# Kernel optimization log

Measured on AMD Instinct MI355X. Metric: run time of the kernel, lower is better.

Reference implementation:

```python
import jax, jax.numpy as jnp
import numpy as np

N_NODES = 50000
N_EDGES = 800000
IN_DIM = 128
HID = 128
NUM_CLASSES = 2


def setup_inputs() -> dict:
    key = jax.random.key(0)
    ks = jax.random.split(key, 16)
    inp = {
        "adj_row": jax.random.randint(ks[0], (N_EDGES,), 0, N_NODES),
        "adj_col": jax.random.randint(ks[1], (N_EDGES,), 0, N_NODES),
        "adj_vals": jax.random.uniform(ks[2], (N_EDGES,), dtype=jnp.float32),
        "input_feature": jax.random.normal(ks[3], (N_NODES, IN_DIM), dtype=jnp.float32),
        "graph_indicator": jax.random.randint(ks[4], (N_NODES,), 0, 64),
        # GCN layer params (kaiming-uniform-ish init; zeros bias like the torch module)
        "W1": jax.random.uniform(ks[5], (IN_DIM, HID), jnp.float32, -1, 1) * np.sqrt(6.0 / IN_DIM),
        "b1": jnp.zeros((HID,), jnp.float32),
        "W2": jax.random.uniform(ks[6], (HID, HID), jnp.float32, -1, 1) * np.sqrt(6.0 / HID),
        "b2": jnp.zeros((HID,), jnp.float32),
        "W3": jax.random.uniform(ks[7], (HID, HID), jnp.float32, -1, 1) * np.sqrt(6.0 / HID),
        "b3": jnp.zeros((HID,), jnp.float32),
        # fc params (torch.nn.Linear default init range)
        "fcW1": jax.random.uniform(ks[8], (3 * HID, HID), jnp.float32, -1, 1) / np.sqrt(3 * HID),
        "fcb1": jax.random.uniform(ks[9], (HID,), jnp.float32, -1, 1) / np.sqrt(3 * HID),
        "fcW2": jax.random.uniform(ks[10], (HID, HID // 2), jnp.float32, -1, 1) / np.sqrt(HID),
        "fcb2": jax.random.uniform(ks[11], (HID // 2,), jnp.float32, -1, 1) / np.sqrt(HID),
        "fcW3": jax.random.uniform(ks[12], (HID // 2, NUM_CLASSES), jnp.float32, -1, 1) / np.sqrt(HID // 2),
        "fcb3": jax.random.uniform(ks[13], (NUM_CLASSES,), jnp.float32, -1, 1) / np.sqrt(HID // 2),
    }
    return inp


def _gcn_layer(row, col, vals, x, W, b, n_nodes):
    # support = X @ W  -> dense GEMM
    support = x @ W
    # sparse.mm(A, support): out[i] = sum_{e: row[e]=i} vals[e] * support[col[e]]
    msgs = support[col] * vals[:, None]  # [E, D] gather + scale
    agg = jax.ops.segment_sum(msgs, row, num_segments=n_nodes)
    return agg + b


def reference(adj_row, adj_col, adj_vals, input_feature, graph_indicator,
              W1, b1, W2, b2, W3, b3, fcW1, fcb1, fcW2, fcb2, fcW3, fcb3):
    n = input_feature.shape[0]
    g1 = jax.nn.relu(_gcn_layer(adj_row, adj_col, adj_vals, input_feature, W1, b1, n))
    g2 = jax.nn.relu(_gcn_layer(adj_row, adj_col, adj_vals, g1, W2, b2, n))
    g3 = jax.nn.relu(_gcn_layer(adj_row, adj_col, adj_vals, g2, W3, b3, n))
    feat = jnp.concatenate([g1, g2, g3], axis=1)  # [N, 3*HID]
    h = jax.nn.relu(feat @ fcW1 + fcb1)
    h = jax.nn.relu(h @ fcW2 + fcb2)
    logits = h @ fcW3 + fcb3
    return logits
```

## Files before the change

### kernel.cpp

```cpp
#include <hip/hip_runtime.h>
#include <hip/hip_bf16.h>

#define N_NODES 50000
#define N_EDGES 800000
#define NB16 3125
#define BCAP16 448
#define REG16 560

static inline int cdiv(int a, int b) { return (a + b - 1) / b; }

typedef __attribute__((ext_vector_type(8))) short short8;
typedef __attribute__((ext_vector_type(4))) float f32x4;

__device__ __forceinline__ float b2f(unsigned short u) {
    union { unsigned int i; float f; } c;
    c.i = ((unsigned int)u) << 16;
    return c.f;
}
__device__ __forceinline__ unsigned short f2bb(float f) {
    __hip_bfloat16 h = __float2bfloat16(f);
    return *(unsigned short*)&h;
}

__device__ __forceinline__ void pack_one(const float* __restrict__ W,
                                         __hip_bfloat16* __restrict__ out,
                                         int K, int N, int t) {
    int lane = t & 63;
    int kc = (t >> 6) % (K / 32);
    int nt = (t >> 6) / (K / 32);
    int kbase = kc * 32 + (lane >> 4) * 8;
    int col = nt * 16 + (lane & 15);
    __hip_bfloat16* dst = out + (size_t)t * 8;
#pragma unroll
    for (int j = 0; j < 8; ++j)
        dst[j] = __float2bfloat16(W[(size_t)(kbase + j) * N + col]);
}

__global__ __launch_bounds__(256)
void stage1_kernel(const int* __restrict__ row, const int* __restrict__ col,
                   const float* __restrict__ vals, int* __restrict__ bcursor,
                   int2* __restrict__ tmp, int E,
                   const float* __restrict__ x, __hip_bfloat16* __restrict__ support,
                   int M,
                   const float* __restrict__ W1, const float* __restrict__ W2,
                   const float* __restrict__ W3, const float* __restrict__ fcW1,
                   const float* __restrict__ fcW2,
                   __hip_bfloat16* __restrict__ pW2, __hip_bfloat16* __restrict__ pW3,
                   __hip_bfloat16* __restrict__ pfcW1, __hip_bfloat16* __restrict__ pfcW2) {
    __shared__ union {
        unsigned short As[64][136];
        struct { int hist[NB16]; int base[NB16]; } bin;
    } sh;
    const int b = blockIdx.x;
    const int tid = threadIdx.x;

    if (b < 196) {
        const int CH = 4096;
        int e0 = b * CH;
        for (int i = tid; i < NB16; i += 256) sh.bin.hist[i] = 0;
        __syncthreads();
        for (int i = tid; i < CH; i += 256) {
            int e = e0 + i;
            if (e < E) atomicAdd(&sh.bin.hist[row[e] >> 4], 1);
        }
        __syncthreads();
        for (int i = tid; i < NB16; i += 256) {
            int c = sh.bin.hist[i];
            sh.bin.base[i] = (c > 0) ? (i * BCAP16 + atomicAdd(&bcursor[i], c)) : 0;
            sh.bin.hist[i] = 0;
        }
        __syncthreads();
        for (int i = tid; i < CH; i += 256) {
            int e = e0 + i;
            if (e < E) {
                int r = row[e];
                int bk = r >> 4;
                int rk = atomicAdd(&sh.bin.hist[bk], 1);
                tmp[sh.bin.base[bk] + rk] = make_int2(((r & 15) << 16) | col[e],
                                                      __float_as_int(vals[e]));
            }
        }
        return;
    }

    if (b < 978) {
        const int wave = tid >> 6;
        const int lane = tid & 63;
        const int ln15 = lane & 15;
        const int quad = lane >> 4;
        const int m0 = (b - 196) * 64;

        short8 bfr[4][2];
#pragma unroll
        for (int kc = 0; kc < 4; ++kc)
#pragma unroll
            for (int h = 0; h < 2; ++h)
#pragma unroll
                for (int j = 0; j < 8; ++j)
                    bfr[kc][h][j] = (short)f2bb(
                        W1[(size_t)(kc * 32 + quad * 8 + j) * 128 + (wave * 2 + h) * 16 + ln15]);

#pragma unroll
        for (int i = 0; i < 4; ++i) {
            int idx = tid + i * 256;
            int r = idx >> 4;
            int c8 = (idx & 15) * 8;
            uint4 pk = {0, 0, 0, 0};
            if (m0 + r < M) {
                const float* src = &x[(size_t)(m0 + r) * 128 + c8];
                float4 a = *(const float4*)src;
                float4 bq = *(const float4*)(src + 4);
                pk.x = f2bb(a.x) | ((unsigned int)f2bb(a.y) << 16);
                pk.y = f2bb(a.z) | ((unsigned int)f2bb(a.w) << 16);
                pk.z = f2bb(bq.x) | ((unsigned int)f2bb(bq.y) << 16);
                pk.w = f2bb(bq.z) | ((unsigned int)f2bb(bq.w) << 16);
            }
            *(uint4*)&sh.As[r][c8] = pk;
        }
        __syncthreads();

        f32x4 acc[4][2];
#pragma unroll
        for (int s = 0; s < 4; ++s)
#pragma unroll
            for (int h = 0; h < 2; ++h) acc[s][h] = (f32x4){0.f, 0.f, 0.f, 0.f};
#pragma unroll
        for (int kc = 0; kc < 4; ++kc) {
            short8 af[4];
#pragma unroll
            for (int s = 0; s < 4; ++s)
                af[s] = *(const short8*)&sh.As[s * 16 + ln15][kc * 32 + quad * 8];
#pragma unroll
            for (int s = 0; s < 4; ++s)
#pragma unroll
                for (int h = 0; h < 2; ++h)
                    acc[s][h] = __builtin_amdgcn_mfma_f32_16x16x32_bf16(
                        af[s], bfr[kc][h], acc[s][h], 0, 0, 0);
        }
#pragma unroll
        for (int s = 0; s < 4; ++s)
#pragma unroll
            for (int h = 0; h < 2; ++h) {
                int cl = (wave * 2 + h) * 16 + ln15;
#pragma unroll
                for (int r = 0; r < 4; ++r) {
                    int rw = m0 + s * 16 + quad * 4 + r;
                    if (rw < M)
                        support[(size_t)rw * 128 + cl] = __float2bfloat16(acc[s][h][r]);
                }
            }
        return;
    }

    int pb = b - 978;
    if (pb < 8)       pack_one(W2,  pW2,  128, 128, pb * 256 + tid);
    else if (pb < 16) pack_one(W3,  pW3,  128, 128, (pb - 8) * 256 + tid);
    else if (pb < 40) pack_one(fcW1, pfcW1, 384, 128, (pb - 16) * 256 + tid);
    else              pack_one(fcW2, pfcW2, 128, 64, (pb - 40) * 256 + tid);
}

__device__ __forceinline__ void accum8(float* acc, long long e, uint4 u) {
    float f = __int_as_float((int)(e >> 32));
    acc[0] += f * b2f((unsigned short)(u.x & 0xffff));
    acc[1] += f * b2f((unsigned short)(u.x >> 16));
    acc[2] += f * b2f((unsigned short)(u.y & 0xffff));
    acc[3] += f * b2f((unsigned short)(u.y >> 16));
    acc[4] += f * b2f((unsigned short)(u.z & 0xffff));
    acc[5] += f * b2f((unsigned short)(u.z >> 16));
    acc[6] += f * b2f((unsigned short)(u.w & 0xffff));
    acc[7] += f * b2f((unsigned short)(u.w >> 16));
}

__device__ __forceinline__ void agg_node(const long long* __restrict__ ep,
                                         const __hip_bfloat16* __restrict__ support,
                                         int p, int end, int g, int j, float* acc) {
#pragma unroll
    for (int k = 0; k < 8; ++k) acc[k] = 0.f;
    long long e0 = 0, e1 = 0;
    uint4 u0 = {0, 0, 0, 0}, u1 = {0, 0, 0, 0};
    bool have = false;
    if (p < end) {
        e0 = ep[p + g];
        e1 = ep[p + 4 + g];
        u0 = *(const uint4*)&support[(size_t)(unsigned int)(e0 & 0xffffffffu) * 128 + j * 8];
        u1 = *(const uint4*)&support[(size_t)(unsigned int)(e1 & 0xffffffffu) * 128 + j * 8];
        p += 8;
        have = true;
    }
    while (p < end) {
        long long f0 = ep[p + g];
        long long f1 = ep[p + 4 + g];
        uint4 w0 = *(const uint4*)&support[(size_t)(unsigned int)(f0 & 0xffffffffu) * 128 + j * 8];
        uint4 w1 = *(const uint4*)&support[(size_t)(unsigned int)(f1 & 0xffffffffu) * 128 + j * 8];
        accum8(acc, e0, u0);
        accum8(acc, e1, u1);
        e0 = f0; u0 = w0; e1 = f1; u1 = w1;
        p += 8;
    }
    if (have) {
        accum8(acc, e0, u0);
        accum8(acc, e1, u1);
    }
#pragma unroll
    for (int k = 0; k < 8; ++k) {
        acc[k] += __shfl_xor(acc[k], 16);
        acc[k] += __shfl_xor(acc[k], 32);
    }
}

__device__ __forceinline__ uint4 pack_row8(const float* acc, float4 b0, float4 b1) {
    unsigned int q0 = (unsigned int)f2bb(fmaxf(acc[0] + b0.x, 0.f))
                    | ((unsigned int)f2bb(fmaxf(acc[1] + b0.y, 0.f)) << 16);
    unsigned int q1 = (unsigned int)f2bb(fmaxf(acc[2] + b0.z, 0.f))
                    | ((unsigned int)f2bb(fmaxf(acc[3] + b0.w, 0.f)) << 16);
    unsigned int q2 = (unsigned int)f2bb(fmaxf(acc[4] + b1.x, 0.f))
                    | ((unsigned int)f2bb(fmaxf(acc[5] + b1.y, 0.f)) << 16);
    unsigned int q3 = (unsigned int)f2bb(fmaxf(acc[6] + b1.z, 0.f))
                    | ((unsigned int)f2bb(fmaxf(acc[7] + b1.w, 0.f)) << 16);
    return (uint4){q0, q1, q2, q3};
}

__global__ __launch_bounds__(256, 8)
void spmm_sort_gemm_kernel(const int2* __restrict__ tmp,
                           const int* __restrict__ bcursor,
                           int2* __restrict__ rowrange, int2* __restrict__ epack,
                           const __hip_bfloat16* __restrict__ support,
                           const float* __restrict__ bias,
                           __hip_bfloat16* __restrict__ gout,
                           const __hip_bfloat16* __restrict__ pW,
                           __hip_bfloat16* __restrict__ Cout,
                           int N) {
    __shared__ unsigned short As[16][136];
    __shared__ int cnt[16];
    __shared__ int cur[16];
    __shared__ int rpos[16];
    const int b = blockIdx.x;
    const int tid = threadIdx.x;
    const int wv = tid >> 6;
    const int l = tid & 63;
    const int g = l >> 4;
    const int j = l & 15;
    const int m0 = b * 16;
    const int r0 = m0;

    if (tid < 16) cnt[tid] = 0;
    __syncthreads();
    int slab = b * BCAP16;
    int send = slab + bcursor[b];
    for (int i = slab + tid; i < send; i += 256)
        atomicAdd(&cnt[tmp[i].x >> 16], 1);
    __syncthreads();
    if (tid == 0) {
        int pos = b * REG16;
#pragma unroll 1
        for (int k = 0; k < 16; ++k) {
            int rc = cnt[k];
            int pc = (rc + 7) & ~7;
            rpos[k] = pos;
            cur[k] = pos;
            rowrange[r0 + k] = make_int2(pos, pos + pc);
            pos += pc;
        }
    }
    __syncthreads();
    for (int i = slab + tid; i < send; i += 256) {
        int2 v = tmp[i];
        int rl = v.x >> 16;
        int pos = atomicAdd(&cur[rl], 1);
        epack[pos] = make_int2(v.x & 0xffff, v.y);
    }
    if (tid < 16) {
        int rc = cnt[tid];
        int pc = (rc + 7) & ~7;
        int pos = rpos[tid];
#pragma unroll 1
        for (int i = pos + rc; i < pos + pc; ++i)
            epack[i] = make_int2(0, 0);
    }
    __syncthreads();

    const long long* ep = (const long long*)epack;
    float4 b0 = *(const float4*)&bias[j * 8];
    float4 b1 = *(const float4*)&bias[j * 8 + 4];
    for (int i = 0; i < 4; ++i) {
        int i0 = wv * 4 + i;
        int ps = rpos[i0];
        int pe = ps + ((cnt[i0] + 7) & ~7);
        float acc[8];
        agg_node(ep, support, ps, pe, g, j, acc);
        if (g == 0) {
            uint4 st = pack_row8(acc, b0, b1);
            *(uint4*)&As[i0][j * 8] = st;
            *(uint4*)&gout[(size_t)(m0 + i0) * 384 + j * 8] = st;
        }
    }
    __syncthreads();

    const int ln15 = l & 15;
    const int quad = l >> 4;
    f32x4 acc2[2];
    acc2[0] = (f32x4){0.f, 0.f, 0.f, 0.f};
    acc2[1] = (f32x4){0.f, 0.f, 0.f, 0.f};
#pragma unroll
    for (int kc = 0; kc < 4; ++kc) {
        short8 af = *(const short8*)&As[ln15][kc * 32 + quad * 8];
#pragma unroll
        for (int h = 0; h < 2; ++h) {
            int nt = wv * 2 + h;
            short8 bf = *(const short8*)&pW[((size_t)(nt * 4 + kc) * 64 + l) * 8];
            acc2[h] = __builtin_amdgcn_mfma_f32_16x16x32_bf16(af, bf, acc2[h], 0, 0, 0);
        }
    }
#pragma unroll
    for (int h = 0; h < 2; ++h) {
        int cl = (wv * 2 + h) * 16 + ln15;
#pragma unroll
        for (int r = 0; r < 4; ++r) {
            int rw = m0 + quad * 4 + r;
            if (rw < N)
                Cout[(size_t)rw * 128 + cl] = __float2bfloat16(acc2[h][r]);
        }
    }
}

__global__ __launch_bounds__(256, 8)
void spmm_gemm_kernel(const int2* __restrict__ rowrange,
                      const int2* __restrict__ epack,
                      const __hip_bfloat16* __restrict__ support,
                      const float* __restrict__ bias,
                      __hip_bfloat16* __restrict__ gout,
                      const __hip_bfloat16* __restrict__ pW,
                      __hip_bfloat16* __restrict__ Cout,
                      int N) {
    __shared__ unsigned short As[16][136];
    const int tid = threadIdx.x;
    const int wv = tid >> 6;
    const int l = tid & 63;
    const int g = l >> 4;
    const int j = l & 15;
    const int m0 = blockIdx.x * 16;
    const long long* ep = (const long long*)epack;
    float4 b0 = *(const float4*)&bias[j * 8];
    float4 b1 = *(const float4*)&bias[j * 8 + 4];

    for (int i = 0; i < 4; ++i) {
        int node = m0 + wv * 4 + i;
        if (node < N) {
            int2 rr = rowrange[node];
            float acc[8];
            agg_node(ep, support, rr.x, rr.y, g, j, acc);
            if (g == 0) {
                uint4 st = pack_row8(acc, b0, b1);
                *(uint4*)&As[wv * 4 + i][j * 8] = st;
                *(uint4*)&gout[(size_t)node * 384 + j * 8] = st;
            }
        } else if (g == 0) {
            *(uint4*)&As[wv * 4 + i][j * 8] = (uint4){0, 0, 0, 0};
        }
    }
    __syncthreads();

    const int ln15 = l & 15;
    const int quad = l >> 4;
    f32x4 acc2[2];
    acc2[0] = (f32x4){0.f, 0.f, 0.f, 0.f};
    acc2[1] = (f32x4){0.f, 0.f, 0.f, 0.f};
#pragma unroll
    for (int kc = 0; kc < 4; ++kc) {
        short8 af = *(const short8*)&As[ln15][kc * 32 + quad * 8];
#pragma unroll
        for (int h = 0; h < 2; ++h) {
            int nt = wv * 2 + h;
            short8 bf = *(const short8*)&pW[((size_t)(nt * 4 + kc) * 64 + l) * 8];
            acc2[h] = __builtin_amdgcn_mfma_f32_16x16x32_bf16(af, bf, acc2[h], 0, 0, 0);
        }
    }
#pragma unroll
    for (int h = 0; h < 2; ++h) {
        int cl = (wv * 2 + h) * 16 + ln15;
#pragma unroll
        for (int r = 0; r < 4; ++r) {
            int rw = m0 + quad * 4 + r;
            if (rw < N)
                Cout[(size_t)rw * 128 + cl] = __float2bfloat16(acc2[h][r]);
        }
    }
}

__global__ __launch_bounds__(256, 8)
void spmm_fc_kernel(const int2* __restrict__ rowrange,
                    const int2* __restrict__ epack,
                    const __hip_bfloat16* __restrict__ support,
                    const float* __restrict__ bias,
                    const __hip_bfloat16* __restrict__ featb,
                    const __hip_bfloat16* __restrict__ pfcW1,
                    const float* __restrict__ fcb1,
                    const __hip_bfloat16* __restrict__ pfcW2,
                    const float* __restrict__ fcb2,
                    const float* __restrict__ fcW3, const float* __restrict__ fcb3,
                    float* __restrict__ out, int N) {
    __shared__ unsigned short As[16][136];
    __shared__ float w3s[128];
    __shared__ float b3s[2];
    const int tid = threadIdx.x;
    const int wv = tid >> 6;
    const int l = tid & 63;
    const int g = l >> 4;
    const int j = l & 15;
    const int m0 = blockIdx.x * 16;
    const long long* ep = (const long long*)epack;
    if (tid < 128) w3s[tid] = fcW3[tid];
    if (tid < 2) b3s[tid] = fcb3[tid];
    float4 b0 = *(const float4*)&bias[j * 8];
    float4 b1 = *(const float4*)&bias[j * 8 + 4];

    for (int i = 0; i < 4; ++i) {
        int node = m0 + wv * 4 + i;
        if (node < N) {
            int2 rr = rowrange[node];
            float acc[8];
            agg_node(ep, support, rr.x, rr.y, g, j, acc);
            if (g == 0)
                *(uint4*)&As[wv * 4 + i][j * 8] = pack_row8(acc, b0, b1);
        } else if (g == 0) {
            *(uint4*)&As[wv * 4 + i][j * 8] = (uint4){0, 0, 0, 0};
        }
    }
    __syncthreads();

    const int ln15 = l & 15;
    const int quad = l >> 4;
    f32x4 acc[2];
    acc[0] = (f32x4){0.f, 0.f, 0.f, 0.f};
    acc[1] = (f32x4){0.f, 0.f, 0.f, 0.f};
#pragma unroll
    for (int step = 0; step < 3; ++step) {
        const int kb = (step == 0) ? 2 : (step - 1);
        if (step != 0) {
            __syncthreads();
            int r = tid >> 4;
            int c8 = (tid & 15) * 8;
            *(uint4*)&As[r][c8] =
                *(const uint4*)&featb[(size_t)(m0 + r) * 384 + kb * 128 + c8];
            __syncthreads();
        }
#pragma unroll
        for (int kc = 0; kc < 4; ++kc) {
            short8 af = *(const short8*)&As[ln15][kc * 32 + quad * 8];
            int kcg = kb * 4 + kc;
#pragma unroll
            for (int h = 0; h < 2; ++h) {
                int nt = wv * 2 + h;
                short8 bf = *(const short8*)&pfcW1[((size_t)(nt * 12 + kcg) * 64 + l) * 8];
                acc[h] = __builtin_amdgcn_mfma_f32_16x16x32_bf16(af, bf, acc[h], 0, 0, 0);
            }
        }
    }
    __syncthreads();
#pragma unroll
    for (int h = 0; h < 2; ++h) {
        int col = (wv * 2 + h) * 16 + ln15;
        float bv = fcb1[col];
#pragma unroll
        for (int r = 0; r < 4; ++r)
            As[quad * 4 + r][col] = f2bb(fmaxf(acc[h][r] + bv, 0.f));
    }
    __syncthreads();

    f32x4 acc2 = (f32x4){0.f, 0.f, 0.f, 0.f};
#pragma unroll
    for (int kc = 0; kc < 4; ++kc) {
        short8 af = *(const short8*)&As[ln15][kc * 32 + quad * 8];
        short8 bfw = *(const short8*)&pfcW2[((size_t)(wv * 4 + kc) * 64 + l) * 8];
        acc2 = __builtin_amdgcn_mfma_f32_16x16x32_bf16(af, bfw, acc2, 0, 0, 0);
    }
    __syncthreads();
    {
        int col2 = wv * 16 + ln15;
        float bv = fcb2[col2];
#pragma unroll
        for (int r = 0; r < 4; ++r)
            As[quad * 4 + r][col2] = f2bb(fmaxf(acc2[r] + bv, 0.f));
    }
    __syncthreads();

    if (tid < 32) {
        int row = tid >> 1, cls = tid & 1;
        int grow = m0 + row;
        if (grow < N) {
            float a = b3s[cls];
#pragma unroll
            for (int k = 0; k < 64; ++k)
                a += b2f(As[row][k]) * w3s[k * 2 + cls];
            out[(size_t)grow * 2 + cls] = a;
        }
    }
}

extern "C" void kernel_launch(void* const* d_in, const int* in_sizes, int n_in,
                              void* d_out, int out_size, void* d_ws, size_t ws_size,
                              hipStream_t stream) {
    const int*   adj_row  = (const int*)d_in[0];
    const int*   adj_col  = (const int*)d_in[1];
    const float* adj_vals = (const float*)d_in[2];
    const float* x        = (const float*)d_in[3];
    const float* W1   = (const float*)d_in[5];
    const float* b1   = (const float*)d_in[6];
    const float* W2   = (const float*)d_in[7];
    const float* b2   = (const float*)d_in[8];
    const float* W3   = (const float*)d_in[9];
    const float* b3   = (const float*)d_in[10];
    const float* fcW1 = (const float*)d_in[11];
    const float* fcb1 = (const float*)d_in[12];
    const float* fcW2 = (const float*)d_in[13];
    const float* fcb2 = (const float*)d_in[14];
    const float* fcW3 = (const float*)d_in[15];
    const float* fcb3 = (const float*)d_in[16];
    float* out = (float*)d_out;

    const int N = N_NODES, E = N_EDGES;
    const int Mpad = 50048;

    char* p = (char*)d_ws;
    auto alloc = [&](size_t bytes) {
        char* q = p;
        p += (bytes + 255) & ~(size_t)255;
        return q;
    };
    __hip_bfloat16* featb    = (__hip_bfloat16*)alloc((size_t)Mpad * 384 * 2);
    __hip_bfloat16* supportb = (__hip_bfloat16*)alloc((size_t)Mpad * 128 * 2);
    __hip_bfloat16* supportc = (__hip_bfloat16*)alloc((size_t)Mpad * 128 * 2);
    __hip_bfloat16* pW2   = (__hip_bfloat16*)alloc(16384 * 2);
    __hip_bfloat16* pW3   = (__hip_bfloat16*)alloc(16384 * 2);
    __hip_bfloat16* pfcW1 = (__hip_bfloat16*)alloc(49152 * 2);
    __hip_bfloat16* pfcW2 = (__hip_bfloat16*)alloc(8192 * 2);
    int2*  rowrange  = (int2*)alloc((size_t)(N + 1) * 8);
    int*   bcursor   = (int*)alloc((size_t)NB16 * 4);
    int2*  epack     = (int2*)alloc((size_t)NB16 * REG16 * 8 + 256);
    int2*  tmp       = (int2*)alloc((size_t)NB16 * BCAP16 * 8);

    hipMemsetAsync(bcursor, 0, (size_t)NB16 * 4, stream);
    stage1_kernel<<<1022, 256, 0, stream>>>(adj_row, adj_col, adj_vals, bcursor, tmp, E,
                                            x, supportb, N,
                                            W1, W2, W3, fcW1, fcW2,
                                            pW2, pW3, pfcW1, pfcW2);

    const int fgrid = NB16;

    spmm_sort_gemm_kernel<<<fgrid, 256, 0, stream>>>(tmp, bcursor, rowrange, epack,
                                                     supportb, b1, featb + 0,
                                                     pW2, supportc, N);
    spmm_gemm_kernel<<<fgrid, 256, 0, stream>>>(rowrange, epack, supportc, b2,
                                                featb + 128, pW3, supportb, N);
    spmm_fc_kernel<<<fgrid, 256, 0, stream>>>(rowrange, epack, supportb, b3,
                                              featb, pfcW1, fcb1, pfcW2, fcb2,
                                              fcW3, fcb3, out, N);
}
```

Baseline: 257.3 us.

## Split edge binning out of fused stage1 kernel into separate launch

Moves the edge-binning work out of the combined stage1 kernel into its own binA kernel and halves each block's edge chunk, which doubles the number of binning blocks. The GEMM/pack kernel no longer carries the large shared-memory union, so it needs less LDS per block and may fit more blocks per CU. The cost is an extra kernel launch, and the binning and the GEMM now run one after the other on the stream instead of overlapping inside a single grid.

```diff
diff --git a/kernel.cpp b/kernel.cpp
--- a/kernel.cpp
+++ b/kernel.cpp
@@ -37,58 +37,57 @@
 }
 
 __global__ __launch_bounds__(256)
-void stage1_kernel(const int* __restrict__ row, const int* __restrict__ col,
-                   const float* __restrict__ vals, int* __restrict__ bcursor,
-                   int2* __restrict__ tmp, int E,
-                   const float* __restrict__ x, __hip_bfloat16* __restrict__ support,
+void binA_kernel(const int* __restrict__ row, const int* __restrict__ col,
+                 const float* __restrict__ vals, int* __restrict__ bcursor,
+                 int2* __restrict__ tmp, int E) {
+    __shared__ int hist[NB16];
+    __shared__ int base[NB16];
+    const int tid = threadIdx.x;
+    const int CH = 2048;
+    int e0 = blockIdx.x * CH;
+    for (int i = tid; i < NB16; i += 256) hist[i] = 0;
+    __syncthreads();
+    for (int i = tid; i < CH; i += 256) {
+        int e = e0 + i;
+        if (e < E) atomicAdd(&hist[row[e] >> 4], 1);
+    }
+    __syncthreads();
+    for (int i = tid; i < NB16; i += 256) {
+        int c = hist[i];
+        base[i] = (c > 0) ? (i * BCAP16 + atomicAdd(&bcursor[i], c)) : 0;
+        hist[i] = 0;
+    }
+    __syncthreads();
+    for (int i = tid; i < CH; i += 256) {
+        int e = e0 + i;
+        if (e < E) {
+            int r = row[e];
+            int bk = r >> 4;
+            int rk = atomicAdd(&hist[bk], 1);
+            tmp[base[bk] + rk] = make_int2(((r & 15) << 16) | col[e],
+                                           __float_as_int(vals[e]));
+        }
+    }
+}
+
+__global__ __launch_bounds__(256)
+void stage1_kernel(const float* __restrict__ x, __hip_bfloat16* __restrict__ support,
                    int M,
                    const float* __restrict__ W1, const float* __restrict__ W2,
                    const float* __restrict__ W3, const float* __restrict__ fcW1,
                    const float* __restrict__ fcW2,
                    __hip_bfloat16* __restrict__ pW2, __hip_bfloat16* __restrict__ pW3,
                    __hip_bfloat16* __restrict__ pfcW1, __hip_bfloat16* __restrict__ pfcW2) {
-    __shared__ union {
-        unsigned short As[64][136];
-        struct { int hist[NB16]; int base[NB16]; } bin;
-    } sh;
+    __shared__ unsigned short As[64][136];
     const int b = blockIdx.x;
     const int tid = threadIdx.x;
 
-    if (b < 196) {
-        const int CH = 4096;
-        int e0 = b * CH;
-        for (int i = tid; i < NB16; i += 256) sh.bin.hist[i] = 0;
-        __syncthreads();
-        for (int i = tid; i < CH; i += 256) {
-            int e = e0 + i;
-            if (e < E) atomicAdd(&sh.bin.hist[row[e] >> 4], 1);
-        }
-        __syncthreads();
-        for (int i = tid; i < NB16; i += 256) {
-            int c = sh.bin.hist[i];
-            sh.bin.base[i] = (c > 0) ? (i * BCAP16 + atomicAdd(&bcursor[i], c)) : 0;
-            sh.bin.hist[i] = 0;
-        }
-        __syncthreads();
-        for (int i = tid; i < CH; i += 256) {
-            int e = e0 + i;
-            if (e < E) {
-                int r = row[e];
-                int bk = r >> 4;
-                int rk = atomicAdd(&sh.bin.hist[bk], 1);
-                tmp[sh.bin.base[bk] + rk] = make_int2(((r & 15) << 16) | col[e],
-                                                      __float_as_int(vals[e]));
-            }
-        }
-        return;
-    }
-
-    if (b < 978) {
+    if (b < 782) {
         const int wave = tid >> 6;
         const int lane = tid & 63;
         const int ln15 = lane & 15;
         const int quad = lane >> 4;
-        const int m0 = (b - 196) * 64;
+        const int m0 = b * 64;
 
         short8 bfr[4][2];
 #pragma unroll
@@ -115,7 +114,7 @@
                 pk.z = f2bb(bq.x) | ((unsigned int)f2bb(bq.y) << 16);
                 pk.w = f2bb(bq.z) | ((unsigned int)f2bb(bq.w) << 16);
             }
-            *(uint4*)&sh.As[r][c8] = pk;
+            *(uint4*)&As[r][c8] = pk;
         }
         __syncthreads();
 
@@ -129,7 +128,7 @@
             short8 af[4];
 #pragma unroll
             for (int s = 0; s < 4; ++s)
-                af[s] = *(const short8*)&sh.As[s * 16 + ln15][kc * 32 + quad * 8];
+                af[s] = *(const short8*)&As[s * 16 + ln15][kc * 32 + quad * 8];
 #pragma unroll
             for (int s = 0; s < 4; ++s)
 #pragma unroll
@@ -152,7 +151,7 @@
         return;
     }
 
-    int pb = b - 978;
+    int pb = b - 782;
     if (pb < 8)       pack_one(W2,  pW2,  128, 128, pb * 256 + tid);
     else if (pb < 16) pack_one(W3,  pW3,  128, 128, (pb - 8) * 256 + tid);
     else if (pb < 40) pack_one(fcW1, pfcW1, 384, 128, (pb - 16) * 256 + tid);
@@ -540,10 +539,11 @@
     int2*  tmp       = (int2*)alloc((size_t)NB16 * BCAP16 * 8);
 
     hipMemsetAsync(bcursor, 0, (size_t)NB16 * 4, stream);
-    stage1_kernel<<<1022, 256, 0, stream>>>(adj_row, adj_col, adj_vals, bcursor, tmp, E,
-                                            x, supportb, N,
-                                            W1, W2, W3, fcW1, fcW2,
-                                            pW2, pW3, pfcW1, pfcW2);
+    binA_kernel<<<cdiv(E, 2048), 256, 0, stream>>>(adj_row, adj_col, adj_vals,
+                                                   bcursor, tmp, E);
+    stage1_kernel<<<826, 256, 0, stream>>>(x, supportb, N,
+                                           W1, W2, W3, fcW1, fcW2,
+                                           pW2, pW3, pfcW1, pfcW2);
 
     const int fgrid = NB16;
 
```

Result: slower. 265.4 us (+3.2%).
